# Kernel optimization log

Measured on AMD Instinct MI355X. Metric: run time of the kernel, lower is better.

## Reference

```python
import jax, jax.numpy as jnp
import numpy as np

V = 255      # v_size
L = 16       # l_size = e_size // v_size (row/col weight of cyclic H)
E = V * L    # e_size
P = 8        # num_permu
B = 1024     # batch
CLIP = 10.0


def _build_indices():
    # Synthetic cyclic H: H[i, j] = 1 iff (j - i) % V in S, |S| = L.
    # Reproduces the torch precompute: pos_cyclic_col / pos_cyclic_row edge
    # orderings and the two edge-permutations between them, plus the
    # num_permu codeword permutations (perma).
    rng = np.random.default_rng(0)
    S = np.sort(rng.choice(V, size=L, replace=False))
    U = S                                  # sorted column offsets per row
    T = np.sort((-S) % V)                  # sorted row offsets per column
    m = np.searchsorted(U, (-T) % V)       # row-ordering slot of each col-slot
    C = np.arange(V)[:, None]
    K = np.arange(L)[None, :]
    R = (T[None, :] + C) % V               # row of k-th edge in column c
    idx_c = (C * L + K).ravel()            # edge index in cyclic-col ordering
    idx_r = (R * L + m[None, :]).ravel()   # same edge in cyclic-row ordering
    rc = np.empty(E, np.int32); rc[idx_c] = idx_r   # cycrowtocyccol
    cr = np.empty(E, np.int32); cr[idx_r] = idx_c   # cyccoltocycrow
    perma = np.stack([rng.permutation(V + 1) for _ in range(P)]).astype(np.int32)
    return rc, cr, perma


def setup_inputs() -> dict:
    key = jax.random.key(0)
    ks = jax.random.split(key, 4)
    rc, cr, perma = _build_indices()
    return {
        "x": jax.random.normal(ks[0], (B, V + 1), jnp.float32),
        "message": jnp.zeros((B, P * E), jnp.float32),
        "oddw_v": jax.random.normal(ks[1], (5, L), jnp.float32),
        "oddw_e": jax.random.normal(ks[2], (5, L, L), jnp.float32),
        "w_e_out": jax.random.normal(ks[3], (L,), jnp.float32),
        "perma": jnp.asarray(perma),
        "rc_idx": jnp.asarray(rc),
        "cr_idx": jnp.asarray(cr),
    }


def reference(x, message, oddw_v, oddw_e, w_e_out, perma, rc_idx, cr_idx):
    Bx = x.shape[0]
    dt = x.dtype
    mask_e = 1.0 - jnp.eye(L, dtype=dt)    # zero diagonal (extrinsic mask)
    idx_v = perma[:, 1:]                   # [P, V]: permute rows, drop row 0

    def odd_layer(ev, wv, we):
        # ev: edge messages [B, P, V, L] in cyclic-col edge ordering
        v0 = x[:, :, None] * wv                                  # [B, V+1, L]
        v_out = v0[:, idx_v, :]                                  # [B, P, V, L]
        e = ev.reshape(Bx, P, E)[:, :, rc_idx].reshape(Bx, P, V, L)
        e_intra = jnp.einsum('bpvl,lm->bpvm', e, we * mask_e)
        return jnp.tanh(0.5 * jnp.clip(v_out + e_intra, -CLIP, CLIP))

    def even_layer(o, flag_clip):
        e = o.reshape(Bx, P, E)[:, :, cr_idx].reshape(Bx, P, V, L)
        e = e + (jnp.abs(e) == 0).astype(dt)            # zeros -> 1
        r = jnp.prod(e, axis=-1, keepdims=True) / e     # leave-one-out product
        if flag_clip:
            r = jnp.clip(r, -CLIP, CLIP)
        return jnp.log((1.0 + r) / (1.0 - r + 1e-9) + 1e-9)

    ev = message.reshape(Bx, P, V, L)
    for t in range(5):                     # 5 BP iterations (fixed depth)
        ev = even_layer(odd_layer(ev, oddw_v[t], oddw_e[t]), t == 0)

    # output layer
    e = ev.reshape(Bx, P, E)[:, :, rc_idx].reshape(Bx, P, V, L)
    eo = jnp.einsum('bpvl,l->bpv', e, w_e_out)          # [B, P, V]
    eo = jnp.pad(eo, ((0, 0), (0, 0), (1, 0)))          # zero at position 0
    idx = jnp.broadcast_to(perma[None].astype(jnp.int32), eo.shape)
    total = jnp.take_along_axis(eo, idx, axis=2).sum(axis=1)  # [B, V+1]
    return x + total
```

## Files before the change

### kernel.cpp

```cpp
#include <hip/hip_runtime.h>

#define V 255
#define L 16
#define E (V*L)
#define P 8
#define CLIPV 10.0f

typedef __attribute__((ext_vector_type(2))) float f32x2;

__device__ __forceinline__ f32x2 splat(float a) { return (f32x2){a, a}; }
__device__ __forceinline__ f32x2 pk_fma(f32x2 a, f32x2 b, f32x2 c) {
    return __builtin_elementwise_fma(a, b, c);
}

__device__ __forceinline__ f32x2 tanh_half_clip_pk(f32x2 s) {
    f32x2 t = __builtin_elementwise_min(
                  __builtin_elementwise_max(s, splat(-CLIPV)), splat(CLIPV));
    f32x2 r;
    float ex = __expf(t.x); r.x = 1.0f - __fdividef(2.0f, ex + 1.0f);
    float ey = __expf(t.y); r.y = 1.0f - __fdividef(2.0f, ey + 1.0f);
    return r;
}

__device__ __forceinline__ int tr_idx(int i) {
    return (i & (L - 1)) * V + (i >> 4);
}

template <int MODE>
__global__ __launch_bounds__(256, 3) void bpp_kernel(
    const float* __restrict__ x,
    const float* __restrict__ oddw_v,
    const float* __restrict__ oddw_e,
    const float* __restrict__ w_e_out,
    const int*   __restrict__ perma,
    const int*   __restrict__ rc_idx,
    const int*   __restrict__ cr_idx,
    float* __restrict__ eo_ws,
    const int* __restrict__ invp,
    float* __restrict__ out)
{
    __shared__ f32x2 S[E];

    const int tid = threadIdx.x;
    const int blk = blockIdx.x;
    const int b  = blk >> 2;
    const int pA = (blk & 3) * 2;
    const int pB = pA + 1;
    const int v = tid;

    f32x2 xv = splat(0.0f);
    if (v < V) {
        const float* xrow = x + b * (V + 1);
        xv.x = xrow[perma[pA * (V + 1) + v + 1]];
        xv.y = xrow[perma[pB * (V + 1) + v + 1]];
    }

    int rci[L], cri[L];
    if (v < V) {
#pragma unroll
        for (int l = 0; l < L; ++l) {
            rci[l] = tr_idx(rc_idx[v * L + l]);
            cri[l] = tr_idx(cr_idx[v * L + l]);
        }
    }

    if (v < V) {
#pragma unroll
        for (int m = 0; m < L; ++m) {
            float w0 = oddw_v[m];
            S[m * V + v] = tanh_half_clip_pk(xv * w0);
        }
    }
    __syncthreads();

#pragma unroll 1
    for (int t = 0; t < 5; ++t) {
        f32x2 e2[L];
        if (v < V) {
#pragma unroll
            for (int l = 0; l < L; ++l) {
                f32x2 q = S[cri[l]];
                q.x = (q.x == 0.0f) ? 1.0f : q.x;
                q.y = (q.y == 0.0f) ? 1.0f : q.y;
                e2[l] = q;
            }
        }
        __syncthreads();

        if (v < V) {
            f32x2 pre[L + 1];
            pre[0] = splat(1.0f);
#pragma unroll
            for (int l = 0; l < L; ++l) pre[l + 1] = pre[l] * e2[l];
            f32x2 suf = splat(1.0f);
#pragma unroll
            for (int l = L - 1; l >= 0; --l) {
                f32x2 r = pre[l] * suf;
                suf = suf * e2[l];
                f32x2 num = r + 1.0f;
                f32x2 den = (1.0f - r) + 1e-9f;
                f32x2 o;
                o.x = __logf(num.x) - __logf(den.x);
                o.y = __logf(num.y) - __logf(den.y);
                S[l * V + v] = o;
            }
        }
        __syncthreads();

        if (t < 4) {
            const float* __restrict__ wm = oddw_e + (t + 1) * (L * L);
            const float* __restrict__ wv = oddw_v + (t + 1) * L;

            f32x2 eg[L];
            if (v < V) {
#pragma unroll
                for (int l = 0; l < L; ++l) eg[l] = S[rci[l]];
            }
            __syncthreads();

            if (v < V) {
                f32x2 s[L];
#pragma unroll
                for (int m = 0; m < L; ++m) s[m] = xv * wv[m];
#pragma unroll
                for (int l = 0; l < L; ++l) {
                    const f32x2 el = eg[l];
#pragma unroll
                    for (int m = 0; m < L; ++m) {
                        if (m != l) {
                            s[m] = pk_fma(el, splat(wm[l * L + m]), s[m]);
                        }
                    }
                }
#pragma unroll
                for (int m = 0; m < L; ++m)
                    S[m * V + v] = tanh_half_clip_pk(s[m]);
            }
            __syncthreads();
        }
    }

    if (v < V) {
        f32x2 d = splat(0.0f);
#pragma unroll
        for (int l = 0; l < L; ++l)
            d = pk_fma(S[rci[l]], splat(w_e_out[l]), d);
        const int uA = blk * 2;
        if (MODE == 0) {
            eo_ws[(size_t)uA * V + v]       = d.x;
            eo_ws[(size_t)(uA + 1) * V + v] = d.y;
        } else {
            int ja = invp[pA * (V + 1) + (v + 1)];
            int jb = invp[pB * (V + 1) + (v + 1)];
            atomicAdd(&out[b * (V + 1) + ja], d.x);
            atomicAdd(&out[b * (V + 1) + jb], d.y);
        }
    }
}

__global__ __launch_bounds__(256) void out_kernel(
    const float* __restrict__ x,
    const float* __restrict__ eo_ws,
    const int* __restrict__ perma,
    float* __restrict__ out)
{
    const int b = blockIdx.x;
    const int j = threadIdx.x;
    float acc = x[b * (V + 1) + j];
#pragma unroll
    for (int p = 0; p < P; ++p) {
        int idx = perma[p * (V + 1) + j];
        if (idx > 0) acc += eo_ws[((size_t)(b * P + p)) * V + (idx - 1)];
    }
    out[b * (V + 1) + j] = acc;
}

__global__ __launch_bounds__(256) void inv_kernel(const int* __restrict__ perma,
                                                  int* __restrict__ invp)
{
    int p = blockIdx.x, j = threadIdx.x;
    invp[p * (V + 1) + perma[p * (V + 1) + j]] = j;
}

__global__ __launch_bounds__(256) void copy_kernel(const float* __restrict__ x,
                                                   float* __restrict__ out, int n)
{
    int i = blockIdx.x * 256 + threadIdx.x;
    if (i < n) out[i] = x[i];
}

extern "C" void kernel_launch(void* const* d_in, const int* in_sizes, int n_in,
                              void* d_out, int out_size, void* d_ws, size_t ws_size,
                              hipStream_t stream)
{
    const float* x       = (const float*)d_in[0];
    const float* oddw_v  = (const float*)d_in[2];
    const float* oddw_e  = (const float*)d_in[3];
    const float* w_e_out = (const float*)d_in[4];
    const int*   perma   = (const int*)d_in[5];
    const int*   rc      = (const int*)d_in[6];
    const int*   cr      = (const int*)d_in[7];
    float* out = (float*)d_out;

    const int Bx = in_sizes[0] / (V + 1);
    const int nunits = Bx * P;
    const size_t need = (size_t)nunits * V * sizeof(float);

    if (ws_size >= need) {
        float* eo = (float*)d_ws;
        hipLaunchKernelGGL((bpp_kernel<0>), dim3(nunits / 2), dim3(256), 0, stream,
                           x, oddw_v, oddw_e, w_e_out, perma, rc, cr,
                           eo, (const int*)nullptr, (float*)nullptr);
        hipLaunchKernelGGL(out_kernel, dim3(Bx), dim3(256), 0, stream,
                           x, eo, perma, out);
    } else {
        int* invp = (int*)d_ws;
        hipLaunchKernelGGL(inv_kernel, dim3(P), dim3(V + 1), 0, stream, perma, invp);
        hipLaunchKernelGGL(copy_kernel, dim3((out_size + 255) / 256), dim3(256), 0, stream,
                           x, out, out_size);
        hipLaunchKernelGGL((bpp_kernel<1>), dim3(nunits / 2), dim3(256), 0, stream,
                           x, oddw_v, oddw_e, w_e_out, perma, rc, cr,
                           (float*)nullptr, invp, out);
    }
}
```

Before: 238.0 us.

## Split each variable node across four threads with double-buffered shared memory

Each variable node is now handled by four threads of a 1024-thread block instead of one, and each thread computes four of the sixteen output edges. Double-buffering shared memory (S0/S1) lets gathers read one buffer while results go to the other, which removes the extra barrier per half-iteration. The leave-one-out product is now the total product divided by the edge value instead of prefix/suffix products, and rc/cr indices are packed into 16-bit pairs to cut registers. The aim is more parallelism and less register pressure. In exchange every thread redundantly gathers all 16 edges for the product, and shared memory per block doubles, which may limit occupancy.

```diff
diff --git a/kernel.cpp b/kernel.cpp
--- a/kernel.cpp
+++ b/kernel.cpp
@@ -22,12 +22,16 @@
     return r;
 }
 
-__device__ __forceinline__ int tr_idx(int i) {
+__device__ __forceinline__ float logratio(float r) {
+    return __logf(__fdividef(1.0f + r, 1.0f - r + 1e-9f) + 1e-9f);
+}
+
+__device__ __forceinline__ int tr_elem(int i) {
     return (i & (L - 1)) * V + (i >> 4);
 }
 
 template <int MODE>
-__global__ __launch_bounds__(256, 3) void bpp_kernel(
+__global__ __launch_bounds__(1024, 8) void bpq_kernel(
     const float* __restrict__ x,
     const float* __restrict__ oddw_v,
     const float* __restrict__ oddw_e,
@@ -39,121 +43,132 @@
     const int* __restrict__ invp,
     float* __restrict__ out)
 {
-    __shared__ f32x2 S[E];
+    __shared__ f32x2 S0[E];
+    __shared__ f32x2 S1[E];
 
     const int tid = threadIdx.x;
+    const int v = tid >> 2;
+    const int q = tid & 3;
     const int blk = blockIdx.x;
     const int b  = blk >> 2;
     const int pA = (blk & 3) * 2;
     const int pB = pA + 1;
-    const int v = tid;
-
+    const bool act = (v < V);
+
+    unsigned pk[L];
     f32x2 xv = splat(0.0f);
-    if (v < V) {
+    if (act) {
+        const int4* rc4 = (const int4*)(rc_idx + v * L);
+        const int4* cr4 = (const int4*)(cr_idx + v * L);
+#pragma unroll
+        for (int i = 0; i < 4; ++i) {
+            int4 a = rc4[i];
+            int4 c = cr4[i];
+            pk[4*i+0] = (unsigned)tr_elem(a.x) | ((unsigned)tr_elem(c.x) << 16);
+            pk[4*i+1] = (unsigned)tr_elem(a.y) | ((unsigned)tr_elem(c.y) << 16);
+            pk[4*i+2] = (unsigned)tr_elem(a.z) | ((unsigned)tr_elem(c.z) << 16);
+            pk[4*i+3] = (unsigned)tr_elem(a.w) | ((unsigned)tr_elem(c.w) << 16);
+        }
         const float* xrow = x + b * (V + 1);
         xv.x = xrow[perma[pA * (V + 1) + v + 1]];
         xv.y = xrow[perma[pB * (V + 1) + v + 1]];
     }
 
-    int rci[L], cri[L];
-    if (v < V) {
-#pragma unroll
-        for (int l = 0; l < L; ++l) {
-            rci[l] = tr_idx(rc_idx[v * L + l]);
-            cri[l] = tr_idx(cr_idx[v * L + l]);
-        }
-    }
-
-    if (v < V) {
-#pragma unroll
-        for (int m = 0; m < L; ++m) {
-            float w0 = oddw_v[m];
-            S[m * V + v] = tanh_half_clip_pk(xv * w0);
-        }
+    if (act) {
+        float4 wv4 = *(const float4*)(oddw_v + 4 * q);
+        S0[(4*q + 0) * V + v] = tanh_half_clip_pk(xv * wv4.x);
+        S0[(4*q + 1) * V + v] = tanh_half_clip_pk(xv * wv4.y);
+        S0[(4*q + 2) * V + v] = tanh_half_clip_pk(xv * wv4.z);
+        S0[(4*q + 3) * V + v] = tanh_half_clip_pk(xv * wv4.w);
     }
     __syncthreads();
 
 #pragma unroll 1
     for (int t = 0; t < 5; ++t) {
-        f32x2 e2[L];
-        if (v < V) {
+        if (act) {
+            f32x2 tp0 = splat(1.0f), tp1 = splat(1.0f);
+            f32x2 tp2 = splat(1.0f), tp3 = splat(1.0f);
+            f32x2 m0, m1, m2, m3;
 #pragma unroll
             for (int l = 0; l < L; ++l) {
-                f32x2 q = S[cri[l]];
-                q.x = (q.x == 0.0f) ? 1.0f : q.x;
-                q.y = (q.y == 0.0f) ? 1.0f : q.y;
-                e2[l] = q;
+                f32x2 qv = S0[pk[l] >> 16];
+                qv.x = (qv.x == 0.0f) ? 1.0f : qv.x;
+                qv.y = (qv.y == 0.0f) ? 1.0f : qv.y;
+                if ((l >> 2) == q) {
+                    if ((l & 3) == 0) m0 = qv;
+                    else if ((l & 3) == 1) m1 = qv;
+                    else if ((l & 3) == 2) m2 = qv;
+                    else m3 = qv;
+                }
+                if ((l & 3) == 0) tp0 = tp0 * qv;
+                else if ((l & 3) == 1) tp1 = tp1 * qv;
+                else if ((l & 3) == 2) tp2 = tp2 * qv;
+                else tp3 = tp3 * qv;
             }
+            f32x2 total = (tp0 * tp1) * (tp2 * tp3);
+            f32x2 o;
+            o.x = logratio(__fdividef(total.x, m0.x));
+            o.y = logratio(__fdividef(total.y, m0.y));
+            S1[(4*q + 0) * V + v] = o;
+            o.x = logratio(__fdividef(total.x, m1.x));
+            o.y = logratio(__fdividef(total.y, m1.y));
+            S1[(4*q + 1) * V + v] = o;
+            o.x = logratio(__fdividef(total.x, m2.x));
+            o.y = logratio(__fdividef(total.y, m2.y));
+            S1[(4*q + 2) * V + v] = o;
+            o.x = logratio(__fdividef(total.x, m3.x));
+            o.y = logratio(__fdividef(total.y, m3.y));
+            S1[(4*q + 3) * V + v] = o;
         }
         __syncthreads();
 
-        if (v < V) {
-            f32x2 pre[L + 1];
-            pre[0] = splat(1.0f);
-#pragma unroll
-            for (int l = 0; l < L; ++l) pre[l + 1] = pre[l] * e2[l];
-            f32x2 suf = splat(1.0f);
-#pragma unroll
-            for (int l = L - 1; l >= 0; --l) {
-                f32x2 r = pre[l] * suf;
-                suf = suf * e2[l];
-                f32x2 num = r + 1.0f;
-                f32x2 den = (1.0f - r) + 1e-9f;
-                f32x2 o;
-                o.x = __logf(num.x) - __logf(den.x);
-                o.y = __logf(num.y) - __logf(den.y);
-                S[l * V + v] = o;
-            }
-        }
-        __syncthreads();
-
         if (t < 4) {
-            const float* __restrict__ wm = oddw_e + (t + 1) * (L * L);
-            const float* __restrict__ wv = oddw_v + (t + 1) * L;
-
-            f32x2 eg[L];
-            if (v < V) {
-#pragma unroll
-                for (int l = 0; l < L; ++l) eg[l] = S[rci[l]];
+            const float* __restrict__ wmrow = oddw_e + (t + 1) * (L * L);
+            if (act) {
+                float4 wv4 = *(const float4*)(oddw_v + (t + 1) * L + 4 * q);
+                f32x2 s0 = xv * wv4.x, s1 = xv * wv4.y;
+                f32x2 s2 = xv * wv4.z, s3 = xv * wv4.w;
+#pragma unroll
+                for (int l = 0; l < L; ++l) {
+                    f32x2 el = S1[pk[l] & 0xffffu];
+                    float4 w4 = *(const float4*)(wmrow + l * L + 4 * q);
+                    float wa = w4.x, wb = w4.y, wc = w4.z, wd = w4.w;
+                    if ((l >> 2) == q) {
+                        if ((l & 3) == 0) wa = 0.0f;
+                        else if ((l & 3) == 1) wb = 0.0f;
+                        else if ((l & 3) == 2) wc = 0.0f;
+                        else wd = 0.0f;
+                    }
+                    s0 = pk_fma(el, splat(wa), s0);
+                    s1 = pk_fma(el, splat(wb), s1);
+                    s2 = pk_fma(el, splat(wc), s2);
+                    s3 = pk_fma(el, splat(wd), s3);
+                }
+                S0[(4*q + 0) * V + v] = tanh_half_clip_pk(s0);
+                S0[(4*q + 1) * V + v] = tanh_half_clip_pk(s1);
+                S0[(4*q + 2) * V + v] = tanh_half_clip_pk(s2);
+                S0[(4*q + 3) * V + v] = tanh_half_clip_pk(s3);
             }
             __syncthreads();
-
-            if (v < V) {
-                f32x2 s[L];
-#pragma unroll
-                for (int m = 0; m < L; ++m) s[m] = xv * wv[m];
-#pragma unroll
-                for (int l = 0; l < L; ++l) {
-                    const f32x2 el = eg[l];
-#pragma unroll
-                    for (int m = 0; m < L; ++m) {
-                        if (m != l) {
-                            s[m] = pk_fma(el, splat(wm[l * L + m]), s[m]);
-                        }
-                    }
-                }
-#pragma unroll
-                for (int m = 0; m < L; ++m)
-                    S[m * V + v] = tanh_half_clip_pk(s[m]);
+        }
+    }
+
+    if (act) {
+        f32x2 d = splat(0.0f);
+#pragma unroll
+        for (int l = 0; l < L; ++l)
+            d = pk_fma(S1[pk[l] & 0xffffu], splat(w_e_out[l]), d);
+        if (q == 0) {
+            const int uA = blk * 2;
+            if (MODE == 0) {
+                eo_ws[(size_t)uA * V + v]       = d.x;
+                eo_ws[(size_t)(uA + 1) * V + v] = d.y;
+            } else {
+                int ja = invp[pA * (V + 1) + (v + 1)];
+                int jb = invp[pB * (V + 1) + (v + 1)];
+                atomicAdd(&out[b * (V + 1) + ja], d.x);
+                atomicAdd(&out[b * (V + 1) + jb], d.y);
             }
-            __syncthreads();
-        }
-    }
-
-    if (v < V) {
-        f32x2 d = splat(0.0f);
-#pragma unroll
-        for (int l = 0; l < L; ++l)
-            d = pk_fma(S[rci[l]], splat(w_e_out[l]), d);
-        const int uA = blk * 2;
-        if (MODE == 0) {
-            eo_ws[(size_t)uA * V + v]       = d.x;
-            eo_ws[(size_t)(uA + 1) * V + v] = d.y;
-        } else {
-            int ja = invp[pA * (V + 1) + (v + 1)];
-            int jb = invp[pB * (V + 1) + (v + 1)];
-            atomicAdd(&out[b * (V + 1) + ja], d.x);
-            atomicAdd(&out[b * (V + 1) + jb], d.y);
         }
     }
 }
@@ -204,11 +219,12 @@
 
     const int Bx = in_sizes[0] / (V + 1);
     const int nunits = Bx * P;
+    const int npairs = nunits / 2;
     const size_t need = (size_t)nunits * V * sizeof(float);
 
     if (ws_size >= need) {
         float* eo = (float*)d_ws;
-        hipLaunchKernelGGL((bpp_kernel<0>), dim3(nunits / 2), dim3(256), 0, stream,
+        hipLaunchKernelGGL((bpq_kernel<0>), dim3(npairs), dim3(1024), 0, stream,
                            x, oddw_v, oddw_e, w_e_out, perma, rc, cr,
                            eo, (const int*)nullptr, (float*)nullptr);
         hipLaunchKernelGGL(out_kernel, dim3(Bx), dim3(256), 0, stream,
@@ -218,7 +234,7 @@
         hipLaunchKernelGGL(inv_kernel, dim3(P), dim3(V + 1), 0, stream, perma, invp);
         hipLaunchKernelGGL(copy_kernel, dim3((out_size + 255) / 256), dim3(256), 0, stream,
                            x, out, out_size);
-        hipLaunchKernelGGL((bpp_kernel<1>), dim3(nunits / 2), dim3(256), 0, stream,
+        hipLaunchKernelGGL((bpq_kernel<1>), dim3(npairs), dim3(1024), 0, stream,
                            x, oddw_v, oddw_e, w_e_out, perma, rc, cr,
                            (float*)nullptr, invp, out);
     }
```

New measurement: 377.2 us. 58.5% more time.

## Use cyclic row structure to share per-row products and keep edge messages in registers

Applied to the files above, without the earlier changes.

The even layer is rewritten so each thread computes one full row product once into a shared TOT array, and each edge's leave-one-out term comes from dividing that total by its own value. The log-ratio is folded into a single log of a quotient instead of two logs, and the odd-layer input stays in registers because the rc gather is replaced by a row lookup. This drops the prefix/suffix product arrays and one gather-plus-barrier per iteration, and launch bounds are raised to 4 waves per SIMD. In exchange, division by the edge value changes the numerics versus the leave-one-out product when values are tiny, and the higher occupancy target may force register spills.

```diff
diff --git a/kernel.cpp b/kernel.cpp
--- a/kernel.cpp
+++ b/kernel.cpp
@@ -22,12 +22,18 @@
     return r;
 }
 
-__device__ __forceinline__ int tr_idx(int i) {
+__device__ __forceinline__ f32x2 zsub(f32x2 o) {
+    o.x = (o.x == 0.0f) ? 1.0f : o.x;
+    o.y = (o.y == 0.0f) ? 1.0f : o.y;
+    return o;
+}
+
+__device__ __forceinline__ int tr_elem(int i) {
     return (i & (L - 1)) * V + (i >> 4);
 }
 
 template <int MODE>
-__global__ __launch_bounds__(256, 3) void bpp_kernel(
+__global__ __launch_bounds__(256, 4) void bpf_kernel(
     const float* __restrict__ x,
     const float* __restrict__ oddw_v,
     const float* __restrict__ oddw_e,
@@ -39,7 +45,8 @@
     const int* __restrict__ invp,
     float* __restrict__ out)
 {
-    __shared__ f32x2 S[E];
+    __shared__ f32x2 OO[E];
+    __shared__ f32x2 TOT[V + 1];
 
     const int tid = threadIdx.x;
     const int blk = blockIdx.x;
@@ -47,104 +54,90 @@
     const int pA = (blk & 3) * 2;
     const int pB = pA + 1;
     const int v = tid;
+    const bool act = (v < V);
 
     f32x2 xv = splat(0.0f);
-    if (v < V) {
+    int crA[L];
+    int rowO[L];
+    if (act) {
         const float* xrow = x + b * (V + 1);
         xv.x = xrow[perma[pA * (V + 1) + v + 1]];
         xv.y = xrow[perma[pB * (V + 1) + v + 1]];
-    }
-
-    int rci[L], cri[L];
-    if (v < V) {
 #pragma unroll
         for (int l = 0; l < L; ++l) {
-            rci[l] = tr_idx(rc_idx[v * L + l]);
-            cri[l] = tr_idx(cr_idx[v * L + l]);
-        }
-    }
-
-    if (v < V) {
-#pragma unroll
-        for (int m = 0; m < L; ++m) {
-            float w0 = oddw_v[m];
-            S[m * V + v] = tanh_half_clip_pk(xv * w0);
-        }
-    }
-    __syncthreads();
+            crA[l]  = tr_elem(cr_idx[v * L + l]);
+            rowO[l] = rc_idx[v * L + l] >> 4;
+        }
+    }
+
+    f32x2 ev[L];
+    if (act) {
+#pragma unroll
+        for (int m = 0; m < L; ++m)
+            ev[m] = zsub(tanh_half_clip_pk(xv * oddw_v[m]));
+    }
 
 #pragma unroll 1
     for (int t = 0; t < 5; ++t) {
-        f32x2 e2[L];
-        if (v < V) {
+        if (act) {
+#pragma unroll
+            for (int m = 0; m < L; ++m) OO[m * V + v] = ev[m];
+        }
+        __syncthreads();
+
+        if (act) {
+            f32x2 t0 = splat(1.0f), t1 = splat(1.0f);
+            f32x2 t2 = splat(1.0f), t3 = splat(1.0f);
+#pragma unroll
+            for (int l = 0; l < L; l += 4) {
+                t0 = t0 * OO[crA[l + 0]];
+                t1 = t1 * OO[crA[l + 1]];
+                t2 = t2 * OO[crA[l + 2]];
+                t3 = t3 * OO[crA[l + 3]];
+            }
+            TOT[v] = (t0 * t1) * (t2 * t3);
+        }
+        __syncthreads();
+
+        if (act) {
 #pragma unroll
             for (int l = 0; l < L; ++l) {
-                f32x2 q = S[cri[l]];
-                q.x = (q.x == 0.0f) ? 1.0f : q.x;
-                q.y = (q.y == 0.0f) ? 1.0f : q.y;
-                e2[l] = q;
+                f32x2 Tl = TOT[rowO[l]];
+                f32x2 e  = ev[l];
+                f32x2 num = e + Tl;
+                f32x2 den = pk_fma(e, splat(1e-9f), e - Tl);
+                f32x2 o;
+                o.x = __logf(__fdividef(num.x, den.x));
+                o.y = __logf(__fdividef(num.y, den.y));
+                ev[l] = o;
             }
-        }
-        __syncthreads();
-
-        if (v < V) {
-            f32x2 pre[L + 1];
-            pre[0] = splat(1.0f);
-#pragma unroll
-            for (int l = 0; l < L; ++l) pre[l + 1] = pre[l] * e2[l];
-            f32x2 suf = splat(1.0f);
-#pragma unroll
-            for (int l = L - 1; l >= 0; --l) {
-                f32x2 r = pre[l] * suf;
-                suf = suf * e2[l];
-                f32x2 num = r + 1.0f;
-                f32x2 den = (1.0f - r) + 1e-9f;
-                f32x2 o;
-                o.x = __logf(num.x) - __logf(den.x);
-                o.y = __logf(num.y) - __logf(den.y);
-                S[l * V + v] = o;
-            }
-        }
-        __syncthreads();
-
-        if (t < 4) {
-            const float* __restrict__ wm = oddw_e + (t + 1) * (L * L);
-            const float* __restrict__ wv = oddw_v + (t + 1) * L;
-
-            f32x2 eg[L];
-            if (v < V) {
-#pragma unroll
-                for (int l = 0; l < L; ++l) eg[l] = S[rci[l]];
-            }
-            __syncthreads();
-
-            if (v < V) {
+            if (t < 4) {
+                const float* __restrict__ wv = oddw_v + (t + 1) * L;
+                const float* __restrict__ wm = oddw_e + (t + 1) * (L * L);
                 f32x2 s[L];
 #pragma unroll
                 for (int m = 0; m < L; ++m) s[m] = xv * wv[m];
 #pragma unroll
                 for (int l = 0; l < L; ++l) {
-                    const f32x2 el = eg[l];
+                    const f32x2 el = ev[l];
 #pragma unroll
                     for (int m = 0; m < L; ++m) {
-                        if (m != l) {
+                        if (m != l)
                             s[m] = pk_fma(el, splat(wm[l * L + m]), s[m]);
-                        }
                     }
                 }
 #pragma unroll
                 for (int m = 0; m < L; ++m)
-                    S[m * V + v] = tanh_half_clip_pk(s[m]);
+                    ev[m] = zsub(tanh_half_clip_pk(s[m]));
             }
-            __syncthreads();
-        }
-    }
-
-    if (v < V) {
+        }
+    }
+
+    if (act) {
         f32x2 d = splat(0.0f);
 #pragma unroll
         for (int l = 0; l < L; ++l)
-            d = pk_fma(S[rci[l]], splat(w_e_out[l]), d);
+            d = pk_fma(ev[l], splat(w_e_out[l]), d);
         const int uA = blk * 2;
         if (MODE == 0) {
             eo_ws[(size_t)uA * V + v]       = d.x;
@@ -204,11 +197,12 @@
 
     const int Bx = in_sizes[0] / (V + 1);
     const int nunits = Bx * P;
+    const int npairs = nunits / 2;
     const size_t need = (size_t)nunits * V * sizeof(float);
 
     if (ws_size >= need) {
         float* eo = (float*)d_ws;
-        hipLaunchKernelGGL((bpp_kernel<0>), dim3(nunits / 2), dim3(256), 0, stream,
+        hipLaunchKernelGGL((bpf_kernel<0>), dim3(npairs), dim3(256), 0, stream,
                            x, oddw_v, oddw_e, w_e_out, perma, rc, cr,
                            eo, (const int*)nullptr, (float*)nullptr);
         hipLaunchKernelGGL(out_kernel, dim3(Bx), dim3(256), 0, stream,
@@ -218,7 +212,7 @@
         hipLaunchKernelGGL(inv_kernel, dim3(P), dim3(V + 1), 0, stream, perma, invp);
         hipLaunchKernelGGL(copy_kernel, dim3((out_size + 255) / 256), dim3(256), 0, stream,
                            x, out, out_size);
-        hipLaunchKernelGGL((bpp_kernel<1>), dim3(nunits / 2), dim3(256), 0, stream,
+        hipLaunchKernelGGL((bpf_kernel<1>), dim3(npairs), dim3(256), 0, stream,
                            x, oddw_v, oddw_e, w_e_out, perma, rc, cr,
                            (float*)nullptr, invp, out);
     }
```

New measurement: 231.7 us. -2.6%, faster.
